# Performance work log

Measured on AMD Instinct MI355X. Metric: run time of the kernel, lower is better.

Reference implementation:

```python
import jax, jax.numpy as jnp
import numpy as np

B, C, H, W = 4, 256, 128, 128
HEADS = 64
HD = C // HEADS  # 4
G = 32           # group norm groups
EPS = 1e-5


def setup_inputs() -> dict:
    key = jax.random.key(0)
    ks = jax.random.split(key, 6)
    x = jax.random.normal(ks[0], (B, C, H, W), dtype=jnp.float32)
    gn_weight = jnp.ones((1, C, 1, 1), dtype=jnp.float32)
    gn_bias = jnp.zeros((1, C, 1, 1), dtype=jnp.float32)
    # 1x1 convs stored as (out_ch, in_ch) matrices
    qkv_w = jax.random.normal(ks[1], (3 * C, C), dtype=jnp.float32) * 0.02
    qkv_b = jax.random.normal(ks[2], (3 * C,), dtype=jnp.float32) * 0.01
    out_w = jax.random.normal(ks[3], (C, C), dtype=jnp.float32) * 0.02
    out_b = jax.random.normal(ks[4], (C,), dtype=jnp.float32) * 0.01
    return {"x": x, "gn_weight": gn_weight, "gn_bias": gn_bias,
            "qkv_w": qkv_w, "qkv_b": qkv_b, "out_w": out_w, "out_b": out_b}


def group_norm(x, weight, bias):
    n, c, h, w = x.shape
    xg = x.reshape(n, G, -1)
    mean = xg.mean(axis=-1, keepdims=True)
    var = jnp.var(xg, axis=-1, keepdims=True, ddof=1)  # torch.var default is unbiased
    xg = (xg - mean) / jnp.sqrt(var + EPS)
    return xg.reshape(n, c, h, w) * weight + bias


def conv1x1(x, w, b):
    # x: (B, Cin, H, W), w: (Cout, Cin)
    return jnp.einsum('bchw,oc->bohw', x, w) + b[None, :, None, None]


def reference(x, gn_weight, gn_bias, qkv_w, qkv_b, out_w, out_b):
    skip = x
    h = group_norm(x, gn_weight, gn_bias)
    qkv = conv1x1(h, qkv_w, qkv_b)                      # (B, 3C, H, W)
    qkv = qkv.reshape(B, HEADS, 3 * HD, H * W)
    q, k, v = jnp.split(qkv, 3, axis=2)                  # each (B, heads, hd, HW)
    scores = jnp.einsum('bhdn,bhen->bhde', q, k) / (HD ** 0.5)  # (B, heads, hd, hd)
    scores = jax.nn.softmax(scores, axis=1)              # softmax over HEADS axis (as in source)
    out = jnp.einsum('bhde,bhen->bhdn', scores, v)       # (B, heads, hd, HW)
    out = out.reshape(B, C, H, W)
    out = conv1x1(out, out_w, out_b)
    return out + skip
```

## Files before the change

### kernel.cpp

```cpp
#include <hip/hip_runtime.h>


constexpr int kB = 4;
constexpr int kC = 256;
constexpr int kHW = 16384;
constexpr int kHeads = 64;
constexpr int kNG = 32;
constexpr int kCPG = 8;
constexpr int kCP1 = 257;
constexpr int kPS = 260;
constexpr float kEPS = 1e-5f;
constexpr int kNSplit = 32;

typedef __attribute__((ext_vector_type(8))) _Float16 f16x8;
typedef __attribute__((ext_vector_type(4))) _Float16 f16x4;
typedef __attribute__((ext_vector_type(4))) float f32x4;

union V8 { f16x8 v; uint4 u; _Float16 h[8]; };

__device__ __forceinline__ void gload16(const void* g, void* l) {
  __builtin_amdgcn_global_load_lds(
      (const __attribute__((address_space(1))) void*)g,
      (__attribute__((address_space(3))) void*)l, 16, 0, 0);
}

constexpr size_t oXT    = 0;
constexpr size_t oXH    = oXT + (size_t)kB * kHW * kC / 2;
constexpr size_t oSpart = oXH + (size_t)kB * kHW * kC / 2;
constexpr size_t oS     = oSpart + (size_t)3 * kB * kNSplit * 128 * 128;
constexpr size_t oSums  = oS + (size_t)kB * kCP1 * kPS;
constexpr size_t oGv    = oSums + (size_t)kB * kC;
constexpr size_t oScore = oGv + (size_t)kB * kC;
constexpr size_t oAq    = oSpart;
constexpr size_t oM     = oXH;
constexpr size_t oGmH   = oXH + (size_t)kB * kC * kPS;

__global__ __launch_bounds__(256) void k0_tr(const float* __restrict__ x,
                                             _Float16* __restrict__ xT,
                                             _Float16* __restrict__ xH,
                                             float* __restrict__ sums) {
  const int nt = blockIdx.x, ct = blockIdx.y, b = blockIdx.z;
  __shared__ float T[64][65];
  const float* xb = x + ((size_t)b * kC + ct * 64) * kHW + nt * 64;
  _Float16* xhb = xH + ((size_t)b * kC + ct * 64) * kHW + nt * 64;
  const int tid = threadIdx.x;
  const int lane = tid & 63;

#pragma unroll
  for (int rep = 0; rep < 2; ++rep) {
    const int r = rep * 32 + (tid >> 3);
    const int c8 = (tid & 7) * 8;
    float4 v0 = *(const float4*)(xb + (size_t)r * kHW + c8);
    float4 v1 = *(const float4*)(xb + (size_t)r * kHW + c8 + 4);
    T[r][c8 + 0] = v0.x; T[r][c8 + 1] = v0.y; T[r][c8 + 2] = v0.z; T[r][c8 + 3] = v0.w;
    T[r][c8 + 4] = v1.x; T[r][c8 + 5] = v1.y; T[r][c8 + 6] = v1.z; T[r][c8 + 7] = v1.w;
    V8 h;
    h.h[0] = (_Float16)v0.x; h.h[1] = (_Float16)v0.y;
    h.h[2] = (_Float16)v0.z; h.h[3] = (_Float16)v0.w;
    h.h[4] = (_Float16)v1.x; h.h[5] = (_Float16)v1.y;
    h.h[6] = (_Float16)v1.z; h.h[7] = (_Float16)v1.w;
    *(uint4*)(xhb + (size_t)r * kHW + c8) = h.u;
    float rs = v0.x + v0.y + v0.z + v0.w + v1.x + v1.y + v1.z + v1.w;
    rs += __shfl_xor(rs, 1);
    rs += __shfl_xor(rs, 2);
    rs += __shfl_xor(rs, 4);
    if ((lane & 7) == 0) atomicAdd(&sums[b * kC + ct * 64 + r], rs);
  }
  __syncthreads();
  const int nl = tid >> 2, cgrp = tid & 3;
  V8 lo, hi;
#pragma unroll
  for (int i = 0; i < 8; ++i)  lo.h[i] = (_Float16)T[cgrp * 16 + i][nl];
#pragma unroll
  for (int i = 0; i < 8; ++i)  hi.h[i] = (_Float16)T[cgrp * 16 + 8 + i][nl];
  _Float16* dst = xT + ((size_t)b * kHW + nt * 64 + nl) * kC + ct * 64 + cgrp * 16;
  *(uint4*)dst = lo.u;
  *(uint4*)(dst + 8) = hi.u;
}

__global__ __launch_bounds__(256) void k1_syrk(const _Float16* __restrict__ xH,
                                               float* __restrict__ Spart) {
  const int tt = blockIdx.x >> 5;
  const int sp = blockIdx.x & 31;
  const int b = blockIdx.y;
  const int ti = (tt == 2) ? 1 : 0;
  const int tj = (tt == 0) ? 0 : 1;
  const bool diag = (ti == tj);
  const _Float16* xb = xH + (size_t)b * kC * kHW;
  const int n0 = sp * (kHW / kNSplit);

  __shared__ __align__(16) _Float16 XI[2][128 * 64];
  __shared__ __align__(16) _Float16 XJ[2][128 * 64];

  const int tid = threadIdx.x;
  const int wave = tid >> 6, lane = tid & 63;
  const int wi = wave >> 1, wj = wave & 1;
  const int lrow = lane & 15, lgq = lane >> 4;
  const int srow = lane >> 3, sslot = lane & 7;

  const _Float16* srcI = xb + (size_t)(ti * 128) * kHW + n0;
  const _Float16* srcJ = xb + (size_t)(tj * 128) * kHW + n0;

  f32x4 acc[16];
#pragma unroll
  for (int i = 0; i < 16; ++i) acc[i] = (f32x4){0.f, 0.f, 0.f, 0.f};

  auto stage = [&](int buf, int nb) {
#pragma unroll
    for (int rep = 0; rep < 4; ++rep) {
      const int rr = rep * 32 + wave * 8 + srow;
      const int g = sslot ^ (rr & 7);
      char* dI = (char*)XI[buf] + (rep * 32 + wave * 8) * 128;
      gload16(srcI + (size_t)rr * kHW + nb + g * 8, dI);
      if (!diag) {
        char* dJ = (char*)XJ[buf] + (rep * 32 + wave * 8) * 128;
        gload16(srcJ + (size_t)rr * kHW + nb + g * 8, dJ);
      }
    }
  };

  stage(0, 0);
  __syncthreads();

  constexpr int NCH = kHW / kNSplit / 64;
  for (int ch = 0; ch < NCH; ++ch) {
    const int buf = ch & 1;
    if (ch + 1 < NCH) stage(buf ^ 1, (ch + 1) * 64);
    const _Float16* XIb = XI[buf];
    const _Float16* XBb = diag ? XI[buf] : XJ[buf];
#pragma unroll
    for (int sub = 0; sub < 2; ++sub) {
      const int gq = sub * 4 + lgq;
      f16x8 afr[4], bfr[4];
#pragma unroll
      for (int ia = 0; ia < 4; ++ia) {
        const int r = wi * 64 + ia * 16 + lrow;
        afr[ia] = *(const f16x8*)((const char*)XIb + (size_t)r * 128 + (((unsigned)(gq ^ (r & 7))) << 4));
      }
#pragma unroll
      for (int jb = 0; jb < 4; ++jb) {
        const int r = wj * 64 + jb * 16 + lrow;
        bfr[jb] = *(const f16x8*)((const char*)XBb + (size_t)r * 128 + (((unsigned)(gq ^ (r & 7))) << 4));
      }
#pragma unroll
      for (int ia = 0; ia < 4; ++ia)
#pragma unroll
        for (int jb = 0; jb < 4; ++jb)
          acc[ia * 4 + jb] = __builtin_amdgcn_mfma_f32_16x16x32_f16(afr[ia], bfr[jb], acc[ia * 4 + jb], 0, 0, 0);
    }
    __syncthreads();
  }
  float* P = Spart + (((size_t)tt * kB + b) * kNSplit + sp) * 16384;
#pragma unroll
  for (int ia = 0; ia < 4; ++ia)
#pragma unroll
    for (int jb = 0; jb < 4; ++jb)
#pragma unroll
      for (int reg = 0; reg < 4; ++reg) {
        const int i = wi * 64 + ia * 16 + lgq * 4 + reg;
        const int j = wj * 64 + jb * 16 + lrow;
        P[(size_t)i * 128 + j] = acc[ia * 4 + jb][reg];
      }
}

__global__ __launch_bounds__(256) void k1r_reduce(const float* __restrict__ Spart,
                                                  float* __restrict__ S) {
  const int blk = blockIdx.x;
  const int tile12 = blk >> 5;
  const int part = blk & 31;
  const int tt = tile12 >> 2, b = tile12 & 3;
  const int rti = (tt == 2) ? 1 : 0;
  const int rtj = (tt == 0) ? 0 : 1;
  const int e0 = part * 512 + threadIdx.x * 2;
  float2 s = {0.f, 0.f};
  const float* base = Spart + ((size_t)tt * kB + b) * kNSplit * 16384 + e0;
#pragma unroll 8
  for (int sp = 0; sp < kNSplit; ++sp) {
    float2 v = *(const float2*)(base + (size_t)sp * 16384);
    s.x += v.x; s.y += v.y;
  }
  const int i = e0 >> 7, j = e0 & 127;
  float* Sb = S + (size_t)b * kCP1 * kPS;
  float* dst = Sb + (size_t)(rti * 128 + i) * kPS + rtj * 128 + j;
  dst[0] = s.x; dst[1] = s.y;
  if (tt == 1) {
    Sb[(size_t)(128 + j + 0) * kPS + i] = s.x;
    Sb[(size_t)(128 + j + 1) * kPS + i] = s.y;
  }
}

__global__ __launch_bounds__(256) void k3a_aq(const float* __restrict__ S,
                                              const float* __restrict__ sums,
                                              const float* __restrict__ gw,
                                              const float* __restrict__ gb,
                                              const float* __restrict__ qkv_w,
                                              const float* __restrict__ qkv_b,
                                              float* __restrict__ Aq) {
  const int ct = blockIdx.x, mt = blockIdx.y, b = blockIdx.z;
  const float* Sb = S + (size_t)b * kCP1 * kPS;
  const float HWf = (float)kHW;
  __shared__ float Wt[32][68];
  __shared__ float Gs[32][68];
  __shared__ float shs[kC], sht[kC], shx[kC], shr[kC];
  __shared__ float meanv[kNG], invv[kNG];
  const int tid = threadIdx.x;
  shx[tid] = sums[b * kC + tid];
  sht[tid] = Sb[(size_t)tid * kPS + tid];
  __syncthreads();
  if (tid < kNG) {
    float sum = 0.f, ssq = 0.f;
#pragma unroll
    for (int k = 0; k < kCPG; ++k) { sum += shx[tid * kCPG + k]; ssq += sht[tid * kCPG + k]; }
    const float n = (float)(kCPG * kHW);
    const float mean = sum / n;
    const float var = (ssq - n * mean * mean) / (n - 1.0f);
    meanv[tid] = mean;
    invv[tid] = rsqrtf(var + kEPS);
  }
  __syncthreads();
  {
    const float sv = gw[tid] * invv[tid / kCPG];
    const float tv = gb[tid] - meanv[tid / kCPG] * sv;
    shs[tid] = sv; sht[tid] = tv;
    shr[tid] = sv * shx[tid] + tv * HWf;
  }
  __syncthreads();
  float acc[16];
#pragma unroll
  for (int i = 0; i < 16; ++i) acc[i] = 0.f;
  const int i0 = (tid & 15) * 4;
  const int j0 = (tid >> 4) * 4;
  const int cp0 = ct * 64;

  for (int cb = 0; cb < kC; cb += 32) {
    int idx = tid;
#pragma unroll
    for (int r = 0; r < 2; ++r) {
      const int m = idx >> 3;
      const int c4 = (idx & 7) * 4;
      const int mg = mt * 64 + m;
      const int row = 12 * (mg >> 2) + (mg & 3);
      float4 v = *(const float4*)(qkv_w + (size_t)row * kC + cb + c4);
      Wt[c4 + 0][m] = v.x; Wt[c4 + 1][m] = v.y; Wt[c4 + 2][m] = v.z; Wt[c4 + 3][m] = v.w;
      idx += 256;
    }
    idx = tid;
#pragma unroll
    for (int r = 0; r < 2; ++r) {
      const int cc = idx >> 4;
      const int n4 = (idx & 15) * 4;
      const int rr = cb + cc;
      const float s_r = shs[rr], t_r = sht[rr], x_r = shx[rr];
      float4 o;
      if (cp0 + n4 < kC) {
        float4 v = *(const float4*)(Sb + (size_t)rr * kPS + cp0 + n4);
        const int cp = cp0 + n4;
        o.x = s_r * (shs[cp + 0] * v.x + sht[cp + 0] * x_r) + t_r * shr[cp + 0];
        o.y = s_r * (shs[cp + 1] * v.y + sht[cp + 1] * x_r) + t_r * shr[cp + 1];
        o.z = s_r * (shs[cp + 2] * v.z + sht[cp + 2] * x_r) + t_r * shr[cp + 2];
        o.w = s_r * (shs[cp + 3] * v.w + sht[cp + 3] * x_r) + t_r * shr[cp + 3];
      } else if (cp0 + n4 == kC) {
        o = (float4){s_r * x_r + t_r * HWf, 0.f, 0.f, 0.f};
      } else {
        o = (float4){0.f, 0.f, 0.f, 0.f};
      }
      *(float4*)&Gs[cc][n4] = o;
      idx += 256;
    }
    __syncthreads();
#pragma unroll
    for (int kk = 0; kk < 32; ++kk) {
      float4 a = *(const float4*)&Wt[kk][i0];
      float4 g = *(const float4*)&Gs[kk][j0];
      acc[0]  += a.x * g.x; acc[1]  += a.x * g.y; acc[2]  += a.x * g.z; acc[3]  += a.x * g.w;
      acc[4]  += a.y * g.x; acc[5]  += a.y * g.y; acc[6]  += a.y * g.z; acc[7]  += a.y * g.w;
      acc[8]  += a.z * g.x; acc[9]  += a.z * g.y; acc[10] += a.z * g.z; acc[11] += a.z * g.w;
      acc[12] += a.w * g.x; acc[13] += a.w * g.y; acc[14] += a.w * g.z; acc[15] += a.w * g.w;
    }
    __syncthreads();
  }
#pragma unroll
  for (int mi = 0; mi < 4; ++mi) {
    const int mg = mt * 64 + i0 + mi;
    const float bias = qkv_b[12 * (mg >> 2) + (mg & 3)];
#pragma unroll
    for (int cj = 0; cj < 4; ++cj) {
      const int cp = cp0 + j0 + cj;
      if (cp < kCP1) {
        const float g256 = (cp < kC) ? shr[cp] : HWf;
        Aq[((size_t)b * kC + mg) * kCP1 + cp] = acc[mi * 4 + cj] + bias * g256;
      }
    }
  }
}

__global__ __launch_bounds__(256) void k3b_scores(const float* __restrict__ Aq,
                                                  const float* __restrict__ qkv_w,
                                                  const float* __restrict__ qkv_b,
                                                  float* __restrict__ score) {
  const int h = blockIdx.x, b = blockIdx.y;
  const int tid = threadIdx.x, wave = tid >> 6, lane = tid & 63;
#pragma unroll
  for (int p = wave; p < 16; p += 4) {
    const int d = p >> 2, e = p & 3;
    const float* aqr = Aq + ((size_t)b * kC + h * 4 + d) * kCP1;
    const int krow = h * 12 + 4 + e;
    float s = 0.f;
#pragma unroll
    for (int it = 0; it < 4; ++it) {
      const int cp = lane + it * 64;
      s += aqr[cp] * qkv_w[(size_t)krow * kC + cp];
    }
    if (lane == 0) s += aqr[256] * qkv_b[krow];
#pragma unroll
    for (int off = 32; off; off >>= 1) s += __shfl_xor(s, off);
    if (lane == 0) score[((size_t)(b * kHeads) + h) * 16 + p] = 0.5f * s;
  }
}

__global__ __launch_bounds__(256) void k45_M(const float* __restrict__ score,
                                             const float* __restrict__ qkv_w,
                                             const float* __restrict__ qkv_b,
                                             float* __restrict__ M) {
  const int b = blockIdx.y;
  const int cidx = blockIdx.x;
  const int h = cidx >> 2, d = cidx & 3;
  __shared__ float sc[64][4];
  __shared__ float mx[4], sm[4];
  const int tid = threadIdx.x;
  {
    const int h2 = tid >> 2, e = tid & 3;
    sc[h2][e] = score[((size_t)(b * kHeads) + h2) * 16 + d * 4 + e];
  }
  __syncthreads();
  const int wave = tid >> 6, lane = tid & 63;
  {
    const float v = sc[lane][wave];
    float m = v;
#pragma unroll
    for (int off = 32; off; off >>= 1) m = fmaxf(m, __shfl_xor(m, off));
    float e2 = expf(v - m);
#pragma unroll
    for (int off = 32; off; off >>= 1) e2 += __shfl_xor(e2, off);
    if (lane == 0) { mx[wave] = m; sm[wave] = e2; }
  }
  __syncthreads();
  const float p0 = expf(sc[h][0] - mx[0]) / sm[0];
  const float p1 = expf(sc[h][1] - mx[1]) / sm[1];
  const float p2 = expf(sc[h][2] - mx[2]) / sm[2];
  const float p3 = expf(sc[h][3] - mx[3]) / sm[3];
  for (int cp = tid; cp < kCP1; cp += 256) {
    float a;
    if (cp < kC) {
      a = p0 * qkv_w[(size_t)(h * 12 + 8 + 0) * kC + cp] +
          p1 * qkv_w[(size_t)(h * 12 + 8 + 1) * kC + cp] +
          p2 * qkv_w[(size_t)(h * 12 + 8 + 2) * kC + cp] +
          p3 * qkv_w[(size_t)(h * 12 + 8 + 3) * kC + cp];
    } else {
      a = p0 * qkv_b[h * 12 + 8 + 0] + p1 * qkv_b[h * 12 + 8 + 1] +
          p2 * qkv_b[h * 12 + 8 + 2] + p3 * qkv_b[h * 12 + 8 + 3];
    }
    M[((size_t)b * kC + cidx) * kPS + cp] = a;
  }
}

__global__ __launch_bounds__(256) void k5b_gemm(const float* __restrict__ M,
                                                const float* __restrict__ out_w,
                                                const float* __restrict__ S,
                                                const float* __restrict__ sums,
                                                const float* __restrict__ gw,
                                                const float* __restrict__ gb,
                                                _Float16* __restrict__ GmH,
                                                float* __restrict__ gvec) {
  const int ct = blockIdx.x, ot = blockIdx.y, b = blockIdx.z;
  const float* Mb = M + (size_t)b * kC * kPS;
  const float* Sb = S + (size_t)b * kCP1 * kPS;
  __shared__ float Wt[32][68];
  __shared__ float Gs[32][68];
  __shared__ float gred[64][17];
  __shared__ float sS[kC], sT[kC];
  __shared__ float meanv[kNG], invv[kNG];
  const int tid = threadIdx.x;
  sS[tid] = sums[b * kC + tid];
  sT[tid] = Sb[(size_t)tid * kPS + tid];
  __syncthreads();
  if (tid < kNG) {
    float sum = 0.f, ssq = 0.f;
#pragma unroll
    for (int k = 0; k < kCPG; ++k) { sum += sS[tid * kCPG + k]; ssq += sT[tid * kCPG + k]; }
    const float n = (float)(kCPG * kHW);
    const float mean = sum / n;
    const float var = (ssq - n * mean * mean) / (n - 1.0f);
    meanv[tid] = mean;
    invv[tid] = rsqrtf(var + kEPS);
  }
  __syncthreads();
  {
    const float xv = sS[tid];
    const float sv = gw[tid] * invv[tid / kCPG];
    sS[tid] = sv;
    sT[tid] = gb[tid] - meanv[tid / kCPG] * sv;
    (void)xv;
  }
  __syncthreads();
  float acc[16];
#pragma unroll
  for (int i = 0; i < 16; ++i) acc[i] = 0.f;
  const int i0 = (tid & 15) * 4;
  const int j0 = (tid >> 4) * 4;
  const int cp0 = ct * 64;

  for (int cb = 0; cb < kC; cb += 32) {
    int idx = tid;
#pragma unroll
    for (int r = 0; r < 2; ++r) {
      const int m = idx >> 3;
      const int c4 = (idx & 7) * 4;
      float4 v = *(const float4*)(out_w + (size_t)(ot * 64 + m) * kC + cb + c4);
      Wt[c4 + 0][m] = v.x; Wt[c4 + 1][m] = v.y; Wt[c4 + 2][m] = v.z; Wt[c4 + 3][m] = v.w;
      idx += 256;
    }
    idx = tid;
#pragma unroll
    for (int r = 0; r < 2; ++r) {
      const int cc = idx >> 4;
      const int n4 = (idx & 15) * 4;
      float4 v = {0.f, 0.f, 0.f, 0.f};
      if (cp0 + n4 < kCP1) v = *(const float4*)(Mb + (size_t)(cb + cc) * kPS + cp0 + n4);
      *(float4*)&Gs[cc][n4] = v;
      idx += 256;
    }
    __syncthreads();
#pragma unroll
    for (int kk = 0; kk < 32; ++kk) {
      float4 a = *(const float4*)&Wt[kk][i0];
      float4 g = *(const float4*)&Gs[kk][j0];
      acc[0]  += a.x * g.x; acc[1]  += a.x * g.y; acc[2]  += a.x * g.z; acc[3]  += a.x * g.w;
      acc[4]  += a.y * g.x; acc[5]  += a.y * g.y; acc[6]  += a.y * g.z; acc[7]  += a.y * g.w;
      acc[8]  += a.z * g.x; acc[9]  += a.z * g.y; acc[10] += a.z * g.z; acc[11] += a.z * g.w;
      acc[12] += a.w * g.x; acc[13] += a.w * g.y; acc[14] += a.w * g.z; acc[15] += a.w * g.w;
    }
    __syncthreads();
  }
  float gpart[4] = {0.f, 0.f, 0.f, 0.f};
#pragma unroll
  for (int mi = 0; mi < 4; ++mi) {
    const int o = ot * 64 + i0 + mi;
#pragma unroll
    for (int cj = 0; cj < 4; ++cj) {
      const int cp = cp0 + j0 + cj;
      const float f = acc[mi * 4 + cj];
      if (cp < kC) {
        GmH[((size_t)b * kC + o) * kC + cp] = (_Float16)(f * sS[cp]);
        gpart[mi] += f * sT[cp];
      } else if (cp == kC) {
        gpart[mi] += f;
      }
    }
  }
#pragma unroll
  for (int mi = 0; mi < 4; ++mi) gred[i0 + mi][tid >> 4] = gpart[mi];
  __syncthreads();
  if (tid < 64) {
    float s = 0.f;
#pragma unroll
    for (int k = 0; k < 16; ++k) s += gred[tid][k];
    atomicAdd(&gvec[b * kC + ot * 64 + tid], s);
  }
}

__global__ __launch_bounds__(256) void k6_final(const _Float16* __restrict__ xT,
                                                const _Float16* __restrict__ GmH,
                                                const float* __restrict__ gvec,
                                                const float* __restrict__ out_b,
                                                const float* __restrict__ x,
                                                float* __restrict__ out) {
  const int nt = blockIdx.x, ot = blockIdx.y, b = blockIdx.z;
  __shared__ __align__(16) char smem[64 * 132 * 4];
  float* Ep = (float*)smem;
  const int tid = threadIdx.x;
  const int wave = tid >> 6, lane = tid & 63;
  const int wo = wave >> 1, wn = wave & 1;
  const int lrow = lane & 15, lgq = lane >> 4;
  const int srow = lane >> 3, sslot = lane & 7;

  const _Float16* xrow = xT + ((size_t)b * kHW + nt * 128) * kC;
  const _Float16* Grow = GmH + (size_t)(b * kC + ot * 128) * kC;

  auto stage = [&](int buf, int cc) {
#pragma unroll
    for (int rep = 0; rep < 4; ++rep) {
      const int rr = rep * 32 + wave * 8 + srow;
      const int g = sslot ^ (rr & 7);
      gload16(xrow + (size_t)rr * kC + cc + g * 8,
              smem + buf * 16384 + (rep * 32 + wave * 8) * 128);
    }
  };

  f32x4 acc[16];
#pragma unroll
  for (int i = 0; i < 16; ++i) acc[i] = (f32x4){0.f, 0.f, 0.f, 0.f};

  stage(0, 0);
  __syncthreads();

  for (int ci = 0; ci < 4; ++ci) {
    const int cc = ci * 64;
    const int buf = ci & 1;
    if (ci < 3) stage(buf ^ 1, cc + 64);
    const char* XB = smem + buf * 16384;
#pragma unroll
    for (int sub = 0; sub < 2; ++sub) {
      const int gq = sub * 4 + lgq;
      f16x8 afr[4], bfr[4];
#pragma unroll
      for (int ia = 0; ia < 4; ++ia) {
        const int r = wo * 64 + ia * 16 + lrow;
        afr[ia] = *(const f16x8*)(Grow + (size_t)r * kC + cc + gq * 8);
      }
#pragma unroll
      for (int jb = 0; jb < 4; ++jb) {
        const int r = wn * 64 + jb * 16 + lrow;
        bfr[jb] = *(const f16x8*)(XB + (size_t)r * 128 + (((unsigned)(gq ^ (r & 7))) << 4));
      }
#pragma unroll
      for (int ia = 0; ia < 4; ++ia)
#pragma unroll
        for (int jb = 0; jb < 4; ++jb)
          acc[ia * 4 + jb] = __builtin_amdgcn_mfma_f32_16x16x32_f16(afr[ia], bfr[jb], acc[ia * 4 + jb], 0, 0, 0);
    }
    __syncthreads();
  }
#pragma unroll
  for (int p = 0; p < 2; ++p) {
    if (wo == p) {
#pragma unroll
      for (int ia = 0; ia < 4; ++ia)
#pragma unroll
        for (int jb = 0; jb < 4; ++jb)
#pragma unroll
          for (int reg = 0; reg < 4; ++reg)
            Ep[(size_t)(ia * 16 + lgq * 4 + reg) * 132 + wn * 64 + jb * 16 + lrow] =
                acc[ia * 4 + jb][reg];
    }
    __syncthreads();
#pragma unroll
    for (int it = 0; it < 8; ++it) {
      const int id = it * 256 + tid;
      const int row = id >> 5, nc = (id & 31) * 4;
      const int o = ot * 128 + p * 64 + row;
      const float gvv = gvec[b * kC + o] + out_b[o];
      float4 e = *(const float4*)&Ep[(size_t)row * 132 + nc];
      const size_t gidx = ((size_t)b * kC + o) * kHW + nt * 128 + nc;
      float4 sk = *(const float4*)&x[gidx];
      float4 res = {e.x + gvv + sk.x, e.y + gvv + sk.y, e.z + gvv + sk.z, e.w + gvv + sk.w};
      *(float4*)&out[gidx] = res;
    }
    __syncthreads();
  }
}

extern "C" void kernel_launch(void* const* d_in, const int* in_sizes, int n_in,
                              void* d_out, int out_size, void* d_ws, size_t ws_size,
                              hipStream_t stream) {
  const float* x    = (const float*)d_in[0];
  const float* gnw  = (const float*)d_in[1];
  const float* gnb  = (const float*)d_in[2];
  const float* qkvw = (const float*)d_in[3];
  const float* qkvb = (const float*)d_in[4];
  const float* outw = (const float*)d_in[5];
  const float* outb = (const float*)d_in[6];
  float* out = (float*)d_out;
  float* ws = (float*)d_ws;

  _Float16* xT   = (_Float16*)(ws + oXT);
  _Float16* xH   = (_Float16*)(ws + oXH);
  float* Spart   = ws + oSpart;
  float* S       = ws + oS;
  float* sums    = ws + oSums;
  float* gv      = ws + oGv;
  float* score   = ws + oScore;
  float* Aq      = ws + oAq;
  float* M       = ws + oM;
  _Float16* GmH  = (_Float16*)(ws + oGmH);

  hipMemsetAsync(sums, 0, (size_t)2 * kB * kC * sizeof(float), stream);
  k0_tr<<<dim3(kHW / 64, kC / 64, kB), 256, 0, stream>>>(x, xT, xH, sums);
  k1_syrk<<<dim3(3 * kNSplit, kB), 256, 0, stream>>>(xH, Spart);
  k1r_reduce<<<dim3(3 * kB * 32), 256, 0, stream>>>(Spart, S);
  k3a_aq<<<dim3(5, 4, kB), 256, 0, stream>>>(S, sums, gnw, gnb, qkvw, qkvb, Aq);
  k3b_scores<<<dim3(kHeads, kB), 256, 0, stream>>>(Aq, qkvw, qkvb, score);
  k45_M<<<dim3(kC, kB), 256, 0, stream>>>(score, qkvw, qkvb, M);
  k5b_gemm<<<dim3(5, 4, kB), 256, 0, stream>>>(M, outw, S, sums, gnw, gnb, GmH, gv);
  k6_final<<<dim3(kHW / 128, kC / 128, kB), 256, 0, stream>>>(xT, GmH, gv, outb, x, out);
}
```

Measured before the change: 247.0 us.

## Replace split-K partial buffer with atomic accumulation and fuse score kernels

The Gram-matrix split-K kernel now accumulates its partial tiles straight into S with float atomics, which removes the separate reduction kernel and the large Spart buffer. The two score kernels (Aq GEMM and the per-head dot products) become one per-head kernel that contracts S with the scaled q weights and then with the v weights, skipping the intermediate Aq matrix. The costs are atomic contention from 32 splits per element, an extra memset of S, and run-to-run nondeterminism in the summation order. Workspace offsets are reorganised so that M and GmH no longer alias xH.

```diff
diff --git a/kernel.cpp b/kernel.cpp
--- a/kernel.cpp
+++ b/kernel.cpp
@@ -26,14 +26,13 @@
 
 constexpr size_t oXT    = 0;
 constexpr size_t oXH    = oXT + (size_t)kB * kHW * kC / 2;
-constexpr size_t oSpart = oXH + (size_t)kB * kHW * kC / 2;
-constexpr size_t oS     = oSpart + (size_t)3 * kB * kNSplit * 128 * 128;
+constexpr size_t oS     = oXH + (size_t)kB * kHW * kC / 2;
 constexpr size_t oSums  = oS + (size_t)kB * kCP1 * kPS;
 constexpr size_t oGv    = oSums + (size_t)kB * kC;
 constexpr size_t oScore = oGv + (size_t)kB * kC;
-constexpr size_t oAq    = oSpart;
-constexpr size_t oM     = oXH;
-constexpr size_t oGmH   = oXH + (size_t)kB * kC * kPS;
+constexpr size_t oEnd   = oScore + (size_t)kB * kHeads * 16;
+constexpr size_t oM     = oEnd;
+constexpr size_t oGmH   = oM + (size_t)kB * kC * kPS;
 
 __global__ __launch_bounds__(256) void k0_tr(const float* __restrict__ x,
                                              _Float16* __restrict__ xT,
@@ -79,7 +78,7 @@
 }
 
 __global__ __launch_bounds__(256) void k1_syrk(const _Float16* __restrict__ xH,
-                                               float* __restrict__ Spart) {
+                                               float* __restrict__ S) {
   const int tt = blockIdx.x >> 5;
   const int sp = blockIdx.x & 31;
   const int b = blockIdx.y;
@@ -150,67 +149,46 @@
     }
     __syncthreads();
   }
-  float* P = Spart + (((size_t)tt * kB + b) * kNSplit + sp) * 16384;
+  float* Sb = S + (size_t)b * kCP1 * kPS;
 #pragma unroll
   for (int ia = 0; ia < 4; ++ia)
 #pragma unroll
     for (int jb = 0; jb < 4; ++jb)
 #pragma unroll
       for (int reg = 0; reg < 4; ++reg) {
-        const int i = wi * 64 + ia * 16 + lgq * 4 + reg;
-        const int j = wj * 64 + jb * 16 + lrow;
-        P[(size_t)i * 128 + j] = acc[ia * 4 + jb][reg];
-      }
-}
-
-__global__ __launch_bounds__(256) void k1r_reduce(const float* __restrict__ Spart,
-                                                  float* __restrict__ S) {
-  const int blk = blockIdx.x;
-  const int tile12 = blk >> 5;
-  const int part = blk & 31;
-  const int tt = tile12 >> 2, b = tile12 & 3;
-  const int rti = (tt == 2) ? 1 : 0;
-  const int rtj = (tt == 0) ? 0 : 1;
-  const int e0 = part * 512 + threadIdx.x * 2;
-  float2 s = {0.f, 0.f};
-  const float* base = Spart + ((size_t)tt * kB + b) * kNSplit * 16384 + e0;
-#pragma unroll 8
-  for (int sp = 0; sp < kNSplit; ++sp) {
-    float2 v = *(const float2*)(base + (size_t)sp * 16384);
-    s.x += v.x; s.y += v.y;
-  }
-  const int i = e0 >> 7, j = e0 & 127;
-  float* Sb = S + (size_t)b * kCP1 * kPS;
-  float* dst = Sb + (size_t)(rti * 128 + i) * kPS + rtj * 128 + j;
-  dst[0] = s.x; dst[1] = s.y;
-  if (tt == 1) {
-    Sb[(size_t)(128 + j + 0) * kPS + i] = s.x;
-    Sb[(size_t)(128 + j + 1) * kPS + i] = s.y;
-  }
-}
-
-__global__ __launch_bounds__(256) void k3a_aq(const float* __restrict__ S,
-                                              const float* __restrict__ sums,
-                                              const float* __restrict__ gw,
-                                              const float* __restrict__ gb,
-                                              const float* __restrict__ qkv_w,
-                                              const float* __restrict__ qkv_b,
-                                              float* __restrict__ Aq) {
-  const int ct = blockIdx.x, mt = blockIdx.y, b = blockIdx.z;
+        const int i = ti * 128 + wi * 64 + ia * 16 + lgq * 4 + reg;
+        const int j = tj * 128 + wj * 64 + jb * 16 + lrow;
+        const float v = acc[ia * 4 + jb][reg];
+        atomicAdd(&Sb[(size_t)i * kPS + j], v);
+        if (tt == 1) atomicAdd(&Sb[(size_t)j * kPS + i], v);
+      }
+}
+
+__global__ __launch_bounds__(256) void k3ab(const float* __restrict__ S,
+                                            const float* __restrict__ sums,
+                                            const float* __restrict__ gw,
+                                            const float* __restrict__ gb,
+                                            const float* __restrict__ qkv_w,
+                                            const float* __restrict__ qkv_b,
+                                            float* __restrict__ score) {
+  const int h = blockIdx.x, b = blockIdx.y;
   const float* Sb = S + (size_t)b * kCP1 * kPS;
   const float HWf = (float)kHW;
-  __shared__ float Wt[32][68];
-  __shared__ float Gs[32][68];
-  __shared__ float shs[kC], sht[kC], shx[kC], shr[kC];
+  __shared__ float shx[kC], shd[kC];
   __shared__ float meanv[kNG], invv[kNG];
+  __shared__ float4 suw[kC];
+  __shared__ float redPQ[4][8];
+  __shared__ float red16[4][16];
   const int tid = threadIdx.x;
+  const int wave = tid >> 6, lane = tid & 63;
+
   shx[tid] = sums[b * kC + tid];
-  sht[tid] = Sb[(size_t)tid * kPS + tid];
+  shd[tid] = Sb[(size_t)tid * kPS + tid];
   __syncthreads();
   if (tid < kNG) {
     float sum = 0.f, ssq = 0.f;
 #pragma unroll
-    for (int k = 0; k < kCPG; ++k) { sum += shx[tid * kCPG + k]; ssq += sht[tid * kCPG + k]; }
+    for (int k = 0; k < kCPG; ++k) { sum += shx[tid * kCPG + k]; ssq += shd[tid * kCPG + k]; }
     const float n = (float)(kCPG * kHW);
     const float mean = sum / n;
     const float var = (ssq - n * mean * mean) / (n - 1.0f);
@@ -218,103 +196,74 @@
     invv[tid] = rsqrtf(var + kEPS);
   }
   __syncthreads();
-  {
-    const float sv = gw[tid] * invv[tid / kCPG];
-    const float tv = gb[tid] - meanv[tid / kCPG] * sv;
-    shs[tid] = sv; sht[tid] = tv;
-    shr[tid] = sv * shx[tid] + tv * HWf;
-  }
-  __syncthreads();
-  float acc[16];
-#pragma unroll
-  for (int i = 0; i < 16; ++i) acc[i] = 0.f;
-  const int i0 = (tid & 15) * 4;
-  const int j0 = (tid >> 4) * 4;
-  const int cp0 = ct * 64;
-
-  for (int cb = 0; cb < kC; cb += 32) {
-    int idx = tid;
-#pragma unroll
-    for (int r = 0; r < 2; ++r) {
-      const int m = idx >> 3;
-      const int c4 = (idx & 7) * 4;
-      const int mg = mt * 64 + m;
-      const int row = 12 * (mg >> 2) + (mg & 3);
-      float4 v = *(const float4*)(qkv_w + (size_t)row * kC + cb + c4);
-      Wt[c4 + 0][m] = v.x; Wt[c4 + 1][m] = v.y; Wt[c4 + 2][m] = v.z; Wt[c4 + 3][m] = v.w;
-      idx += 256;
-    }
-    idx = tid;
-#pragma unroll
-    for (int r = 0; r < 2; ++r) {
-      const int cc = idx >> 4;
-      const int n4 = (idx & 15) * 4;
-      const int rr = cb + cc;
-      const float s_r = shs[rr], t_r = sht[rr], x_r = shx[rr];
-      float4 o;
-      if (cp0 + n4 < kC) {
-        float4 v = *(const float4*)(Sb + (size_t)rr * kPS + cp0 + n4);
-        const int cp = cp0 + n4;
-        o.x = s_r * (shs[cp + 0] * v.x + sht[cp + 0] * x_r) + t_r * shr[cp + 0];
-        o.y = s_r * (shs[cp + 1] * v.y + sht[cp + 1] * x_r) + t_r * shr[cp + 1];
-        o.z = s_r * (shs[cp + 2] * v.z + sht[cp + 2] * x_r) + t_r * shr[cp + 2];
-        o.w = s_r * (shs[cp + 3] * v.w + sht[cp + 3] * x_r) + t_r * shr[cp + 3];
-      } else if (cp0 + n4 == kC) {
-        o = (float4){s_r * x_r + t_r * HWf, 0.f, 0.f, 0.f};
-      } else {
-        o = (float4){0.f, 0.f, 0.f, 0.f};
-      }
-      *(float4*)&Gs[cc][n4] = o;
-      idx += 256;
-    }
-    __syncthreads();
-#pragma unroll
-    for (int kk = 0; kk < 32; ++kk) {
-      float4 a = *(const float4*)&Wt[kk][i0];
-      float4 g = *(const float4*)&Gs[kk][j0];
-      acc[0]  += a.x * g.x; acc[1]  += a.x * g.y; acc[2]  += a.x * g.z; acc[3]  += a.x * g.w;
-      acc[4]  += a.y * g.x; acc[5]  += a.y * g.y; acc[6]  += a.y * g.z; acc[7]  += a.y * g.w;
-      acc[8]  += a.z * g.x; acc[9]  += a.z * g.y; acc[10] += a.z * g.z; acc[11] += a.z * g.w;
-      acc[12] += a.w * g.x; acc[13] += a.w * g.y; acc[14] += a.w * g.z; acc[15] += a.w * g.w;
-    }
-    __syncthreads();
-  }
-#pragma unroll
-  for (int mi = 0; mi < 4; ++mi) {
-    const int mg = mt * 64 + i0 + mi;
-    const float bias = qkv_b[12 * (mg >> 2) + (mg & 3)];
-#pragma unroll
-    for (int cj = 0; cj < 4; ++cj) {
-      const int cp = cp0 + j0 + cj;
-      if (cp < kCP1) {
-        const float g256 = (cp < kC) ? shr[cp] : HWf;
-        Aq[((size_t)b * kC + mg) * kCP1 + cp] = acc[mi * 4 + cj] + bias * g256;
-      }
-    }
-  }
-}
-
-__global__ __launch_bounds__(256) void k3b_scores(const float* __restrict__ Aq,
-                                                  const float* __restrict__ qkv_w,
-                                                  const float* __restrict__ qkv_b,
-                                                  float* __restrict__ score) {
-  const int h = blockIdx.x, b = blockIdx.y;
-  const int tid = threadIdx.x, wave = tid >> 6, lane = tid & 63;
-#pragma unroll
-  for (int p = wave; p < 16; p += 4) {
-    const int d = p >> 2, e = p & 3;
-    const float* aqr = Aq + ((size_t)b * kC + h * 4 + d) * kCP1;
-    const int krow = h * 12 + 4 + e;
-    float s = 0.f;
-#pragma unroll
-    for (int it = 0; it < 4; ++it) {
-      const int cp = lane + it * 64;
-      s += aqr[cp] * qkv_w[(size_t)krow * kC + cp];
-    }
-    if (lane == 0) s += aqr[256] * qkv_b[krow];
-#pragma unroll
-    for (int off = 32; off; off >>= 1) s += __shfl_xor(s, off);
-    if (lane == 0) score[((size_t)(b * kHeads) + h) * 16 + p] = 0.5f * s;
+  const float s_c = gw[tid] * invv[tid / kCPG];
+  const float t_c = gb[tid] - meanv[tid / kCPG] * s_c;
+  const float x_c = shx[tid];
+  const float r_c = s_c * x_c + t_c * HWf;
+
+  const float u0 = qkv_w[(size_t)(h * 12 + 0) * kC + tid];
+  const float u1 = qkv_w[(size_t)(h * 12 + 1) * kC + tid];
+  const float u2 = qkv_w[(size_t)(h * 12 + 2) * kC + tid];
+  const float u3 = qkv_w[(size_t)(h * 12 + 3) * kC + tid];
+  const float v0 = qkv_w[(size_t)(h * 12 + 4) * kC + tid];
+  const float v1 = qkv_w[(size_t)(h * 12 + 5) * kC + tid];
+  const float v2 = qkv_w[(size_t)(h * 12 + 6) * kC + tid];
+  const float v3 = qkv_w[(size_t)(h * 12 + 7) * kC + tid];
+  suw[tid] = make_float4(u0 * s_c, u1 * s_c, u2 * s_c, u3 * s_c);
+
+  float p[8] = {u0 * s_c * x_c, u1 * s_c * x_c, u2 * s_c * x_c, u3 * s_c * x_c,
+                u0 * t_c, u1 * t_c, u2 * t_c, u3 * t_c};
+#pragma unroll
+  for (int i = 0; i < 8; ++i)
+#pragma unroll
+    for (int off = 32; off; off >>= 1) p[i] += __shfl_xor(p[i], off);
+  if (lane == 0) {
+#pragma unroll
+    for (int i = 0; i < 8; ++i) redPQ[wave][i] = p[i];
+  }
+  __syncthreads();
+  float P[4], Qp[4];
+#pragma unroll
+  for (int d = 0; d < 4; ++d) {
+    P[d]  = redPQ[0][d] + redPQ[1][d] + redPQ[2][d] + redPQ[3][d];
+    Qp[d] = redPQ[0][4 + d] + redPQ[1][4 + d] + redPQ[2][4 + d] + redPQ[3][4 + d]
+            + qkv_b[h * 12 + d];
+  }
+
+  float sd0 = 0.f, sd1 = 0.f, sd2 = 0.f, sd3 = 0.f;
+#pragma unroll 8
+  for (int c = 0; c < kC; ++c) {
+    const float Sval = Sb[(size_t)c * kPS + tid];
+    const float4 w = suw[c];
+    sd0 += w.x * Sval; sd1 += w.y * Sval; sd2 += w.z * Sval; sd3 += w.w * Sval;
+  }
+  float wd[4];
+#pragma unroll
+  for (int d = 0; d < 4; ++d) {
+    const float sdv = (d == 0) ? sd0 : (d == 1) ? sd1 : (d == 2) ? sd2 : sd3;
+    wd[d] = s_c * sdv + t_c * P[d] + r_c * Qp[d];
+  }
+  const float sv[4] = {v0, v1, v2, v3};
+  float pr[16];
+#pragma unroll
+  for (int d = 0; d < 4; ++d)
+#pragma unroll
+    for (int e = 0; e < 4; ++e) pr[d * 4 + e] = wd[d] * sv[e];
+#pragma unroll
+  for (int i = 0; i < 16; ++i)
+#pragma unroll
+    for (int off = 32; off; off >>= 1) pr[i] += __shfl_xor(pr[i], off);
+  if (lane == 0) {
+#pragma unroll
+    for (int i = 0; i < 16; ++i) red16[wave][i] = pr[i];
+  }
+  __syncthreads();
+  if (tid < 16) {
+    const int d = tid >> 2, e = tid & 3;
+    float tot = red16[0][tid] + red16[1][tid] + red16[2][tid] + red16[3][tid];
+    const float w256 = P[d] + HWf * Qp[d];
+    tot += w256 * qkv_b[h * 12 + 4 + e];
+    score[((size_t)(b * kHeads) + h) * 16 + tid] = 0.5f * tot;
   }
 }
 
@@ -396,11 +345,9 @@
   }
   __syncthreads();
   {
-    const float xv = sS[tid];
     const float sv = gw[tid] * invv[tid / kCPG];
     sS[tid] = sv;
     sT[tid] = gb[tid] - meanv[tid / kCPG] * sv;
-    (void)xv;
   }
   __syncthreads();
   float acc[16];
@@ -575,21 +522,18 @@
 
   _Float16* xT   = (_Float16*)(ws + oXT);
   _Float16* xH   = (_Float16*)(ws + oXH);
-  float* Spart   = ws + oSpart;
   float* S       = ws + oS;
   float* sums    = ws + oSums;
   float* gv      = ws + oGv;
   float* score   = ws + oScore;
-  float* Aq      = ws + oAq;
   float* M       = ws + oM;
   _Float16* GmH  = (_Float16*)(ws + oGmH);
 
   hipMemsetAsync(sums, 0, (size_t)2 * kB * kC * sizeof(float), stream);
+  hipMemsetAsync(S, 0, (size_t)kB * kCP1 * kPS * sizeof(float), stream);
   k0_tr<<<dim3(kHW / 64, kC / 64, kB), 256, 0, stream>>>(x, xT, xH, sums);
-  k1_syrk<<<dim3(3 * kNSplit, kB), 256, 0, stream>>>(xH, Spart);
-  k1r_reduce<<<dim3(3 * kB * 32), 256, 0, stream>>>(Spart, S);
-  k3a_aq<<<dim3(5, 4, kB), 256, 0, stream>>>(S, sums, gnw, gnb, qkvw, qkvb, Aq);
-  k3b_scores<<<dim3(kHeads, kB), 256, 0, stream>>>(Aq, qkvw, qkvb, score);
+  k1_syrk<<<dim3(3 * kNSplit, kB), 256, 0, stream>>>(xH, S);
+  k3ab<<<dim3(kHeads, kB), 256, 0, stream>>>(S, sums, gnw, gnb, qkvw, qkvb, score);
   k45_M<<<dim3(kC, kB), 256, 0, stream>>>(score, qkvw, qkvb, M);
   k5b_gemm<<<dim3(5, 4, kB), 256, 0, stream>>>(M, outw, S, sums, gnw, gnb, GmH, gv);
   k6_final<<<dim3(kHW / 128, kC / 128, kB), 256, 0, stream>>>(xT, GmH, gv, outb, x, out);
```

Result: slower. 312.4 us (+26.5%).
